# Kernel optimization log

Hardware: AMD Instinct MI355X
Metric: run time of the kernel (lower is better)

The kernel has to match this reference:

```python
import jax, jax.numpy as jnp
import numpy as np

TEMP = 1.0
EPS = 1e-6


def trop_linear(x, w, b, temp=TEMP):
    # x: (..., in), w: (out, in) -> (..., out)
    # y_i = temp * logsumexp_j((w_ij + x_j)/temp) + b_i  (soft tropical / max-plus)
    z = x[..., None, :] + w  # (..., out, in)
    y = temp * jax.nn.logsumexp(z / temp, axis=-1)
    return y + b


def trop_layernorm(x, weight, bias, eps=EPS):
    n = x.shape[-1]
    # torch.median returns the lower of the two middle elements for even n
    med = jnp.sort(x, axis=-1)[..., (n - 1) // 2][..., None]
    q75 = jnp.quantile(x, 0.75, axis=-1, keepdims=True)
    q25 = jnp.quantile(x, 0.25, axis=-1, keepdims=True)
    iqr = jnp.maximum(q75 - q25, eps)
    return (x - med) / iqr * weight + bias


def setup_inputs() -> dict:
    key = jax.random.key(0)
    ks = jax.random.split(key, 8)
    B, D_IN, D_H, D_OUT = 1024, 512, 512, 256
    return {
        "x": jax.random.normal(ks[0], (B, D_IN), dtype=jnp.float32),
        "w1": 0.1 * jax.random.normal(ks[1], (D_H, D_IN), dtype=jnp.float32),
        "b1": jnp.zeros((D_H,), dtype=jnp.float32),
        "ln1_w": jnp.ones((D_H,), dtype=jnp.float32),
        "ln1_b": jnp.zeros((D_H,), dtype=jnp.float32),
        "w2": 0.1 * jax.random.normal(ks[2], (D_H, D_H), dtype=jnp.float32),
        "b2": jnp.zeros((D_H,), dtype=jnp.float32),
        "ln2_w": jnp.ones((D_H,), dtype=jnp.float32),
        "ln2_b": jnp.zeros((D_H,), dtype=jnp.float32),
        "w3": 0.1 * jax.random.normal(ks[3], (D_OUT, D_H), dtype=jnp.float32),
        "b3": jnp.zeros((D_OUT,), dtype=jnp.float32),
    }


def reference(x, w1, b1, ln1_w, ln1_b, w2, b2, ln2_w, ln2_b, w3, b3):
    h = trop_linear(x, w1, b1)
    h = trop_layernorm(h, ln1_w, ln1_b)
    h = jnp.maximum(h, 0.0)  # TropicalActivation('relu', threshold=0)
    h = trop_linear(h, w2, b2)
    h = trop_layernorm(h, ln2_w, ln2_b)
    h = jnp.maximum(h, 0.0)
    return trop_linear(h, w3, b3)
```

## Files before the change

kernel.cpp:

```cpp
#include <hip/hip_runtime.h>
#include <math.h>


typedef float v4f __attribute__((ext_vector_type(4)));

#define LN64f 4.1588830833596715f

__device__ __forceinline__ int pk4_fp8(float a, float b, float c, float d) {
    int p = __builtin_amdgcn_cvt_pk_fp8_f32(a, b, 0, 0);
    p = __builtin_amdgcn_cvt_pk_fp8_f32(c, d, p, 1);
    return p;
}

__global__ __launch_bounds__(256) void prep_frag(const float* __restrict__ w1,
                                                 const float* __restrict__ w2,
                                                 const float* __restrict__ w3,
                                                 const float* __restrict__ x,
                                                 uint8_t* __restrict__ Ew,
                                                 uint8_t* __restrict__ Ax) {
    int u = blockIdx.x * 256 + threadIdx.x;
    int lane = u & 63, t = (u >> 6) & 15, S = u >> 10;
    int r = lane & 15, q = lane >> 4;
    const float* m; int tile; uint8_t* dst; float sc;
    if (S < 32)      { m = w1; tile = S;      dst = Ew;          sc = 1.0f; }
    else if (S < 64) { m = w2; tile = S - 32; dst = Ew + 262144; sc = 1.0f; }
    else if (S < 80) { m = w3; tile = S - 64; dst = Ew + 524288; sc = 1.0f; }
    else             { m = x;  tile = S - 80; dst = Ax;          sc = 4.0f; }
    const float* src = m + (tile * 16 + r) * 512 + t * 32 + q * 8;
    float4 a = *reinterpret_cast<const float4*>(src);
    float4 b = *reinterpret_cast<const float4*>(src + 4);
    int2 o;
    o.x = pk4_fp8(sc * __expf(a.x), sc * __expf(a.y),
                  sc * __expf(a.z), sc * __expf(a.w));
    o.y = pk4_fp8(sc * __expf(b.x), sc * __expf(b.y),
                  sc * __expf(b.z), sc * __expf(b.w));
    *reinterpret_cast<int2*>(dst + (tile * 16 + t) * 512 + lane * 8) = o;
}

__device__ __forceinline__ v4f gemm_k512_1(const uint8_t* __restrict__ ap,
                                           const uint8_t* __restrict__ bp) {
    long areg[16];
    long bb[8];
#pragma unroll
    for (int t = 0; t < 16; ++t)
        areg[t] = *reinterpret_cast<const long*>(ap + t * 512);
#pragma unroll
    for (int p = 0; p < 8; ++p)
        bb[p] = *reinterpret_cast<const long*>(bp + p * 512);
    v4f acc = (v4f){0.f, 0.f, 0.f, 0.f};
#pragma unroll
    for (int t = 0; t < 16; ++t) {
        long a = areg[t];
        long bcur = bb[t & 7];
        if (t < 8)
            bb[t & 7] = *reinterpret_cast<const long*>(bp + (t + 8) * 512);
        acc = __builtin_amdgcn_mfma_f32_16x16x32_fp8_fp8(a, bcur, acc, 0, 0, 0);
    }
    return acc;
}

__global__ __launch_bounds__(256) void gemm_h(const uint8_t* __restrict__ Af,
                                              const uint8_t* __restrict__ Bf,
                                              const float* __restrict__ bias,
                                              float* __restrict__ h) {
    int W = blockIdx.x * 4 + (threadIdx.x >> 6);
    int lane = threadIdx.x & 63;
    int m = W >> 5, n16 = W & 31;
    int r = lane & 15, q = lane >> 4;
    v4f acc = gemm_k512_1(Af + m * 8192 + lane * 8,
                          Bf + n16 * 8192 + lane * 8);
    int col = n16 * 16 + r;
    float bv = bias[col];
#pragma unroll
    for (int tt = 0; tt < 4; ++tt)
        h[(m * 16 + q * 4 + tt) * 512 + col] = __logf(acc[tt]) + bv;
}

__global__ __launch_bounds__(256) void gemm_out(const uint8_t* __restrict__ Af,
                                                const uint8_t* __restrict__ Bf,
                                                const float* __restrict__ b3,
                                                const float* __restrict__ crow,
                                                float* __restrict__ out) {
    int W = blockIdx.x * 4 + (threadIdx.x >> 6);
    int lane = threadIdx.x & 63;
    int m = W >> 4, n16 = W & 15;
    int r = lane & 15, q = lane >> 4;
    v4f acc = gemm_k512_1(Af + m * 8192 + lane * 8,
                          Bf + n16 * 8192 + lane * 8);
    int col = n16 * 16 + r;
    float bv = b3[col] - LN64f;
#pragma unroll
    for (int tt = 0; tt < 4; ++tt) {
        int row = m * 16 + q * 4 + tt;
        out[row * 256 + col] = __logf(acc[tt]) + crow[row] + bv;
    }
}

__global__ __launch_bounds__(256) void ln_rows(const float* __restrict__ h,
                                               const float* __restrict__ lw,
                                               const float* __restrict__ lb,
                                               uint8_t* __restrict__ Aout,
                                               float* __restrict__ crow) {
    int w = threadIdx.x >> 6, lane = threadIdx.x & 63;
    int rho = blockIdx.x * 4 + w;

    const float4* lw4 = reinterpret_cast<const float4*>(lw + lane * 8);
    const float4* lb4 = reinterpret_cast<const float4*>(lb + lane * 8);
    float4 wa = lw4[0], wb = lw4[1], ba = lb4[0], bbv = lb4[1];

    float hv[8], v[8];
    {
        const float* hp = h + rho * 512 + lane * 8;
        float4 a = *reinterpret_cast<const float4*>(hp);
        float4 b = *reinterpret_cast<const float4*>(hp + 4);
        hv[0] = a.x; hv[1] = a.y; hv[2] = a.z; hv[3] = a.w;
        hv[4] = b.x; hv[5] = b.y; hv[6] = b.z; hv[7] = b.w;
#pragma unroll
        for (int j = 0; j < 8; ++j) v[j] = hv[j];
    }
#pragma clang loop unroll(disable)
    for (int k = 2; k <= 512; k <<= 1) {
#pragma clang loop unroll(disable)
        for (int jj = 256; jj > 0; jj >>= 1) {
            if (jj >= k) continue;
            if (jj >= 8) {
                int lm = jj >> 3;
#pragma unroll
                for (int j = 0; j < 8; ++j) {
                    float pv = __shfl_xor(v[j], lm);
                    bool up = ((((lane << 3) | j) & k) == 0);
                    bool low = ((lane & lm) == 0);
                    v[j] = (up == low) ? fminf(v[j], pv) : fmaxf(v[j], pv);
                }
            } else if (jj == 4) {
#pragma unroll
                for (int j = 0; j < 4; ++j) {
                    bool up = ((((lane << 3) | j) & k) == 0);
                    float a = v[j], c = v[j + 4];
                    float lo = fminf(a, c), hi = fmaxf(a, c);
                    v[j] = up ? lo : hi;
                    v[j + 4] = up ? hi : lo;
                }
            } else if (jj == 2) {
#pragma unroll
                for (int jb = 0; jb < 8; jb += 4)
#pragma unroll
                    for (int j0 = 0; j0 < 2; ++j0) {
                        int j = jb + j0;
                        bool up = ((((lane << 3) | j) & k) == 0);
                        float a = v[j], c = v[j + 2];
                        float lo = fminf(a, c), hi = fmaxf(a, c);
                        v[j] = up ? lo : hi;
                        v[j + 2] = up ? hi : lo;
                    }
            } else {
#pragma unroll
                for (int j = 0; j < 8; j += 2) {
                    bool up = ((((lane << 3) | j) & k) == 0);
                    float a = v[j], c = v[j + 1];
                    float lo = fminf(a, c), hi = fmaxf(a, c);
                    v[j] = up ? lo : hi;
                    v[j + 1] = up ? hi : lo;
                }
            }
        }
    }
    float s127 = __shfl(v[7], 15);
    float s128 = __shfl(v[0], 16);
    float med  = __shfl(v[7], 31);
    float s383 = __shfl(v[7], 47);
    float s384 = __shfl(v[0], 48);
    float q25 = s127 + 0.75f * (s128 - s127);
    float q75 = s383 + 0.25f * (s384 - s383);
    float inv = 1.0f / fmaxf(q75 - q25, 1e-6f);

    float y[8], cm = 0.0f;
    {
        float lwv[8] = {wa.x, wa.y, wa.z, wa.w, wb.x, wb.y, wb.z, wb.w};
        float lbv[8] = {ba.x, ba.y, ba.z, ba.w, bbv.x, bbv.y, bbv.z, bbv.w};
#pragma unroll
        for (int j = 0; j < 8; ++j) {
            y[j] = fmaxf((hv[j] - med) * inv * lwv[j] + lbv[j], 0.0f);
            cm = fmaxf(cm, y[j]);
        }
    }
#pragma unroll
    for (int s = 32; s > 0; s >>= 1) cm = fmaxf(cm, __shfl_xor(cm, s));
    {
        float e[8];
#pragma unroll
        for (int j = 0; j < 8; ++j) e[j] = 64.0f * __expf(y[j] - cm);
        int2 o;
        o.x = pk4_fp8(e[0], e[1], e[2], e[3]);
        o.y = pk4_fp8(e[4], e[5], e[6], e[7]);
        uint8_t* dst = Aout + ((rho >> 4) * 16 + (lane >> 2)) * 512
                            + ((lane & 3) * 16 + (rho & 15)) * 8;
        *reinterpret_cast<int2*>(dst) = o;
    }
    if (lane == 0) crow[rho] = cm;
}

extern "C" void kernel_launch(void* const* d_in, const int* in_sizes, int n_in,
                              void* d_out, int out_size, void* d_ws, size_t ws_size,
                              hipStream_t stream) {
    const float* x    = (const float*)d_in[0];
    const float* w1   = (const float*)d_in[1];
    const float* b1   = (const float*)d_in[2];
    const float* ln1w = (const float*)d_in[3];
    const float* ln1b = (const float*)d_in[4];
    const float* w2   = (const float*)d_in[5];
    const float* b2   = (const float*)d_in[6];
    const float* ln2w = (const float*)d_in[7];
    const float* ln2b = (const float*)d_in[8];
    const float* w3   = (const float*)d_in[9];
    const float* b3   = (const float*)d_in[10];
    float* out = (float*)d_out;

    uint8_t* ws = (uint8_t*)d_ws;
    uint8_t* Ew   = ws;
    uint8_t* A1   = ws + (1u << 20);
    uint8_t* A2   = ws + (1u << 20) + 524288;
    uint8_t* A3   = ws + (2u << 20);
    float*   h    = (float*)(ws + (2u << 20) + 524288);
    float*   crow = (float*)(ws + (5u << 20));

    prep_frag<<<576, 256, 0, stream>>>(w1, w2, w3, x, Ew, A1);
    gemm_h<<<512, 256, 0, stream>>>(A1, Ew, b1, h);
    ln_rows<<<256, 256, 0, stream>>>(h, ln1w, ln1b, A2, crow);
    gemm_h<<<512, 256, 0, stream>>>(A2, Ew + 262144, b2, h);
    ln_rows<<<256, 256, 0, stream>>>(h, ln2w, ln2b, A3, crow);
    gemm_out<<<256, 256, 0, stream>>>(A3, Ew + 524288, b3, crow, out);
}
```

Baseline: 111.6 us.

## Fuse six kernel launches into one cooperative persistent kernel with grid syncs

Merges the weight/input prep, both hidden GEMMs, both layernorm passes and the output GEMM into a single cooperative kernel of 512 blocks, separating the stages with grid.sync(). The aim is to remove the launch overhead and inter-kernel gaps of six small launches. In exchange, layernorm and the final GEMM now use only half the waves per block, and every grid-wide barrier has its own cost. The cooperative launch also requires all 512 blocks to be co-resident, which __launch_bounds__(256,2) is meant to help with.

```diff
diff --git a/kernel.cpp b/kernel.cpp
--- a/kernel.cpp
+++ b/kernel.cpp
@@ -1,5 +1,8 @@
 #include <hip/hip_runtime.h>
+#include <hip/hip_cooperative_groups.h>
 #include <math.h>
+
+namespace cg = cooperative_groups;
 
 
 typedef float v4f __attribute__((ext_vector_type(4)));
@@ -10,31 +13,6 @@
     int p = __builtin_amdgcn_cvt_pk_fp8_f32(a, b, 0, 0);
     p = __builtin_amdgcn_cvt_pk_fp8_f32(c, d, p, 1);
     return p;
-}
-
-__global__ __launch_bounds__(256) void prep_frag(const float* __restrict__ w1,
-                                                 const float* __restrict__ w2,
-                                                 const float* __restrict__ w3,
-                                                 const float* __restrict__ x,
-                                                 uint8_t* __restrict__ Ew,
-                                                 uint8_t* __restrict__ Ax) {
-    int u = blockIdx.x * 256 + threadIdx.x;
-    int lane = u & 63, t = (u >> 6) & 15, S = u >> 10;
-    int r = lane & 15, q = lane >> 4;
-    const float* m; int tile; uint8_t* dst; float sc;
-    if (S < 32)      { m = w1; tile = S;      dst = Ew;          sc = 1.0f; }
-    else if (S < 64) { m = w2; tile = S - 32; dst = Ew + 262144; sc = 1.0f; }
-    else if (S < 80) { m = w3; tile = S - 64; dst = Ew + 524288; sc = 1.0f; }
-    else             { m = x;  tile = S - 80; dst = Ax;          sc = 4.0f; }
-    const float* src = m + (tile * 16 + r) * 512 + t * 32 + q * 8;
-    float4 a = *reinterpret_cast<const float4*>(src);
-    float4 b = *reinterpret_cast<const float4*>(src + 4);
-    int2 o;
-    o.x = pk4_fp8(sc * __expf(a.x), sc * __expf(a.y),
-                  sc * __expf(a.z), sc * __expf(a.w));
-    o.y = pk4_fp8(sc * __expf(b.x), sc * __expf(b.y),
-                  sc * __expf(b.z), sc * __expf(b.w));
-    *reinterpret_cast<int2*>(dst + (tile * 16 + t) * 512 + lane * 8) = o;
 }
 
 __device__ __forceinline__ v4f gemm_k512_1(const uint8_t* __restrict__ ap,
@@ -59,51 +37,12 @@
     return acc;
 }
 
-__global__ __launch_bounds__(256) void gemm_h(const uint8_t* __restrict__ Af,
-                                              const uint8_t* __restrict__ Bf,
-                                              const float* __restrict__ bias,
-                                              float* __restrict__ h) {
-    int W = blockIdx.x * 4 + (threadIdx.x >> 6);
-    int lane = threadIdx.x & 63;
-    int m = W >> 5, n16 = W & 31;
-    int r = lane & 15, q = lane >> 4;
-    v4f acc = gemm_k512_1(Af + m * 8192 + lane * 8,
-                          Bf + n16 * 8192 + lane * 8);
-    int col = n16 * 16 + r;
-    float bv = bias[col];
-#pragma unroll
-    for (int tt = 0; tt < 4; ++tt)
-        h[(m * 16 + q * 4 + tt) * 512 + col] = __logf(acc[tt]) + bv;
-}
-
-__global__ __launch_bounds__(256) void gemm_out(const uint8_t* __restrict__ Af,
-                                                const uint8_t* __restrict__ Bf,
-                                                const float* __restrict__ b3,
-                                                const float* __restrict__ crow,
-                                                float* __restrict__ out) {
-    int W = blockIdx.x * 4 + (threadIdx.x >> 6);
-    int lane = threadIdx.x & 63;
-    int m = W >> 4, n16 = W & 15;
-    int r = lane & 15, q = lane >> 4;
-    v4f acc = gemm_k512_1(Af + m * 8192 + lane * 8,
-                          Bf + n16 * 8192 + lane * 8);
-    int col = n16 * 16 + r;
-    float bv = b3[col] - LN64f;
-#pragma unroll
-    for (int tt = 0; tt < 4; ++tt) {
-        int row = m * 16 + q * 4 + tt;
-        out[row * 256 + col] = __logf(acc[tt]) + crow[row] + bv;
-    }
-}
-
-__global__ __launch_bounds__(256) void ln_rows(const float* __restrict__ h,
-                                               const float* __restrict__ lw,
-                                               const float* __restrict__ lb,
-                                               uint8_t* __restrict__ Aout,
-                                               float* __restrict__ crow) {
-    int w = threadIdx.x >> 6, lane = threadIdx.x & 63;
-    int rho = blockIdx.x * 4 + w;
-
+__device__ __forceinline__ void ln_one_row(int rho, int lane,
+                                           const float* __restrict__ h,
+                                           const float* __restrict__ lw,
+                                           const float* __restrict__ lb,
+                                           uint8_t* __restrict__ Aout,
+                                           float* __restrict__ crow) {
     const float4* lw4 = reinterpret_cast<const float4*>(lw + lane * 8);
     const float4* lb4 = reinterpret_cast<const float4*>(lb + lane * 8);
     float4 wa = lw4[0], wb = lw4[1], ba = lb4[0], bbv = lb4[1];
@@ -198,6 +137,90 @@
         *reinterpret_cast<int2*>(dst) = o;
     }
     if (lane == 0) crow[rho] = cm;
+}
+
+__global__ __launch_bounds__(256, 2) void trop_all(
+    const float* __restrict__ x,
+    const float* __restrict__ w1, const float* __restrict__ b1,
+    const float* __restrict__ ln1w, const float* __restrict__ ln1b,
+    const float* __restrict__ w2, const float* __restrict__ b2,
+    const float* __restrict__ ln2w, const float* __restrict__ ln2b,
+    const float* __restrict__ w3, const float* __restrict__ b3,
+    uint8_t* __restrict__ Ew, uint8_t* __restrict__ A1,
+    uint8_t* __restrict__ A2, uint8_t* __restrict__ A3,
+    float* __restrict__ h, float* __restrict__ crow,
+    float* __restrict__ out)
+{
+    cg::grid_group grid = cg::this_grid();
+    const int tid = threadIdx.x, blk = blockIdx.x;
+    const int lane = tid & 63, w = tid >> 6;
+    const int r = lane & 15, q = lane >> 4;
+
+    for (int u = blk * 256 + tid; u < 147456; u += 131072) {
+        int ul = u & 63, t = (u >> 6) & 15, S = u >> 10;
+        int ur = ul & 15, uq = ul >> 4;
+        const float* m; int tile; uint8_t* dst; float sc;
+        if (S < 32)      { m = w1; tile = S;      dst = Ew;          sc = 1.0f; }
+        else if (S < 64) { m = w2; tile = S - 32; dst = Ew + 262144; sc = 1.0f; }
+        else if (S < 80) { m = w3; tile = S - 64; dst = Ew + 524288; sc = 1.0f; }
+        else             { m = x;  tile = S - 80; dst = A1;          sc = 4.0f; }
+        const float* src = m + (tile * 16 + ur) * 512 + t * 32 + uq * 8;
+        float4 a = *reinterpret_cast<const float4*>(src);
+        float4 b = *reinterpret_cast<const float4*>(src + 4);
+        int2 o;
+        o.x = pk4_fp8(sc * __expf(a.x), sc * __expf(a.y),
+                      sc * __expf(a.z), sc * __expf(a.w));
+        o.y = pk4_fp8(sc * __expf(b.x), sc * __expf(b.y),
+                      sc * __expf(b.z), sc * __expf(b.w));
+        *reinterpret_cast<int2*>(dst + (tile * 16 + t) * 512 + ul * 8) = o;
+    }
+    grid.sync();
+
+    {
+        int W = blk * 4 + w;
+        int m = W >> 5, n16 = W & 31;
+        v4f acc = gemm_k512_1(A1 + m * 8192 + lane * 8,
+                              Ew + n16 * 8192 + lane * 8);
+        int col = n16 * 16 + r;
+        float bv = b1[col];
+#pragma unroll
+        for (int tt = 0; tt < 4; ++tt)
+            h[(m * 16 + q * 4 + tt) * 512 + col] = __logf(acc[tt]) + bv;
+    }
+    grid.sync();
+
+    if (w < 2) ln_one_row(blk * 2 + w, lane, h, ln1w, ln1b, A2, crow);
+    grid.sync();
+
+    {
+        int W = blk * 4 + w;
+        int m = W >> 5, n16 = W & 31;
+        v4f acc = gemm_k512_1(A2 + m * 8192 + lane * 8,
+                              Ew + 262144 + n16 * 8192 + lane * 8);
+        int col = n16 * 16 + r;
+        float bv = b2[col];
+#pragma unroll
+        for (int tt = 0; tt < 4; ++tt)
+            h[(m * 16 + q * 4 + tt) * 512 + col] = __logf(acc[tt]) + bv;
+    }
+    grid.sync();
+
+    if (w < 2) ln_one_row(blk * 2 + w, lane, h, ln2w, ln2b, A3, crow);
+    grid.sync();
+
+    if (w < 2) {
+        int W3 = blk * 2 + w;
+        int m = W3 >> 4, n16 = W3 & 15;
+        v4f acc = gemm_k512_1(A3 + m * 8192 + lane * 8,
+                              Ew + 524288 + n16 * 8192 + lane * 8);
+        int col = n16 * 16 + r;
+        float bv = b3[col] - LN64f;
+#pragma unroll
+        for (int tt = 0; tt < 4; ++tt) {
+            int row = m * 16 + q * 4 + tt;
+            out[row * 256 + col] = __logf(acc[tt]) + crow[row] + bv;
+        }
+    }
 }
 
 extern "C" void kernel_launch(void* const* d_in, const int* in_sizes, int n_in,
@@ -224,10 +247,8 @@
     float*   h    = (float*)(ws + (2u << 20) + 524288);
     float*   crow = (float*)(ws + (5u << 20));
 
-    prep_frag<<<576, 256, 0, stream>>>(w1, w2, w3, x, Ew, A1);
-    gemm_h<<<512, 256, 0, stream>>>(A1, Ew, b1, h);
-    ln_rows<<<256, 256, 0, stream>>>(h, ln1w, ln1b, A2, crow);
-    gemm_h<<<512, 256, 0, stream>>>(A2, Ew + 262144, b2, h);
-    ln_rows<<<256, 256, 0, stream>>>(h, ln2w, ln2b, A3, crow);
-    gemm_out<<<256, 256, 0, stream>>>(A3, Ew + 524288, b3, crow, out);
-}
+    void* args[] = {&x, &w1, &b1, &ln1w, &ln1b, &w2, &b2, &ln2w, &ln2b,
+                    &w3, &b3, &Ew, &A1, &A2, &A3, &h, &crow, &out};
+    hipLaunchCooperativeKernel((void*)trop_all, dim3(512), dim3(256),
+                               args, 0, stream);
+}
```

Result: slower. 400.4 us (+258.7%).
